# Kernel tuning notes

Measured on AMD Instinct MI355X. Metric: run time of the kernel, lower is better.

## Reference

```python
import jax, jax.numpy as jnp
import numpy as np

U1 = 512
U2 = 512
BATCH = 8192
INPUT_DIM = (U1 + U2) * 3  # 3072
UNITS = U2 * 3             # 1536


def _build_mask():
    """Replicates the block-structured random 0/1 unit_diags construction.

    Unit blocks (rows): [0,U2), [U2,2U2), [2U2,3U2).
    Input blocks (cols): ds1,ds2,ds3 of width U1 each, then stn1,stn2,stn3 of width U2.
    Each (unit-block, input-block) pair has a fixed Bernoulli keep-probability
    derived from the original randint(2)/randint(4) logic.
    """
    rng = np.random.default_rng(0)
    col_edges = [0, U1, 2 * U1, 3 * U1, 3 * U1 + U2, 3 * U1 + 2 * U2, 3 * U1 + 3 * U2]
    # keep-probabilities per unit-block (rows) x input-block (cols)
    probs = [
        [1.0, 0.5, 0.0, 1.0, 0.5, 0.0],   # units [0, U2)
        [0.5, 0.75, 0.5, 0.5, 0.75, 0.5], # units [U2, 2U2): randint(4)>0 -> p=0.75
        [0.0, 0.5, 1.0, 0.0, 0.5, 1.0],   # units [2U2, 3U2)
    ]
    p = np.zeros((UNITS, INPUT_DIM), dtype=np.float32)
    for ub in range(3):
        for j in range(6):
            p[ub * U2:(ub + 1) * U2, col_edges[j]:col_edges[j + 1]] = probs[ub][j]
    mask = (rng.random((UNITS, INPUT_DIM)) < p).astype(np.float32)
    return mask


def setup_inputs() -> dict:
    key = jax.random.key(0)
    k1, k2 = jax.random.split(key)
    x = jax.random.normal(k1, (BATCH, INPUT_DIM), dtype=jnp.float32)
    # w_init = uniform(0, 0.01), non-negative constrained
    w = jax.random.uniform(k2, (INPUT_DIM, UNITS), dtype=jnp.float32, minval=0.0, maxval=0.01)
    # gpi_bias = [0, 0] -> bias initialized to zeros
    b = jnp.zeros((UNITS,), dtype=jnp.float32)
    mask = jnp.asarray(_build_mask())  # (UNITS, INPUT_DIM), fixed 0/1 constants
    return {"x": x, "w": w, "b": b, "mask": mask}


def reference(x, w, b, mask):
    # Original: p[b,u,:] = mask[u,:] * x[b,:] ;  f = diag_part(p @ w) + b
    # => f[b,u] = sum_i mask[u,i] * x[b,i] * w[i,u] + b[u]
    # Collapses to a masked linear: x @ (mask.T * w) + b
    return x @ (mask.T * w) + b
```

## Files before the change

kernel.cpp:

```cpp
#include <hip/hip_runtime.h>
#include <stdint.h>

#define MDIM 8192
#define NDIM 1536
#define KDIM 3072

#define BM 128
#define BN 128
#define BK 64

#define NMB ((KDIM / 64) * (NDIM / 64))
#define NCVT ((MDIM * KDIM / 4) / 256)

typedef unsigned short u16;
typedef float  f32x4  __attribute__((ext_vector_type(4)));
typedef __bf16 bf16x8 __attribute__((ext_vector_type(8)));

__device__ __forceinline__ u16 f2bf(float f) {
    union { float f; unsigned int u; } v; v.f = f;
    unsigned int u = v.u;
    return (u16)((u + 0x7fffu + ((u >> 16) & 1u)) >> 16);
}

__global__ void prep_kernel(const float* __restrict__ w, const float* __restrict__ mask,
                            u16* __restrict__ Bt,
                            const float4* __restrict__ x, ushort4* __restrict__ xb) {
    const int t = threadIdx.x;
    if (blockIdx.x < NMB) {
        __shared__ float sw[64][65];
        const int kb = blockIdx.x % (KDIM / 64);
        const int nb = blockIdx.x / (KDIM / 64);
        const int k0 = kb * 64, n0 = nb * 64;
        {
            const int c4 = t & 15;
            const int r  = t >> 4;
#pragma unroll
            for (int rr = 0; rr < 4; ++rr) {
                int row = rr * 16 + r;
                float4 v = *(const float4*)&w[(size_t)(k0 + row) * NDIM + n0 + c4 * 4];
                sw[row][c4 * 4 + 0] = v.x;
                sw[row][c4 * 4 + 1] = v.y;
                sw[row][c4 * 4 + 2] = v.z;
                sw[row][c4 * 4 + 3] = v.w;
            }
        }
        __syncthreads();
        {
            const int n  = t >> 2;
            const int ks = (t & 3) * 16;
#pragma unroll
            for (int j = 0; j < 4; ++j) {
                int k = ks + j * 4;
                float4 mv = *(const float4*)&mask[(size_t)(n0 + n) * KDIM + k0 + k];
                ushort4 o;
                o.x = f2bf(mv.x * sw[k + 0][n]);
                o.y = f2bf(mv.y * sw[k + 1][n]);
                o.z = f2bf(mv.z * sw[k + 2][n]);
                o.w = f2bf(mv.w * sw[k + 3][n]);
                *(ushort4*)&Bt[(size_t)(n0 + n) * KDIM + k0 + k] = o;
            }
        }
    } else {
        int i = (blockIdx.x - NMB) * 256 + t;
        float4 v = x[i];
        ushort4 o;
        o.x = f2bf(v.x); o.y = f2bf(v.y); o.z = f2bf(v.z); o.w = f2bf(v.w);
        xb[i] = o;
    }
}

__device__ __forceinline__ void gload_lds16(const void* g, void* l) {
    __builtin_amdgcn_global_load_lds(
        (const __attribute__((address_space(1))) unsigned int*)g,
        (__attribute__((address_space(3))) unsigned int*)l, 16, 0, 0);
}

#define PLANE (128 * 32)

__global__ void gemm_kernel(const u16* __restrict__ A,
                            const u16* __restrict__ B,
                            const float* __restrict__ bias,
                            float* __restrict__ C) {
    __shared__ u16 sA[2 * PLANE];
    __shared__ u16 sB[2 * PLANE];

    const int tid  = threadIdx.x;
    const int wave = tid >> 6;
    const int lane = tid & 63;

    const int bx = blockIdx.x % (NDIM / BN);
    const int by = blockIdx.x / (NDIM / BN);
    const int m0 = by * BM, n0 = bx * BN;

    const int srow = lane >> 2;
    const int scol = ((lane & 3) ^ ((lane >> 3) & 3)) * 8;

    const int wm = (wave >> 1) * 64;
    const int wn = (wave & 1) * 64;
    const int fr = lane & 15;
    const int fq = lane >> 4;
    const int fsw = (fq ^ ((fr >> 1) & 3)) * 8;

    f32x4 acc[4][4] = {};

    const u16* gA0 = A + (size_t)(m0 + wave * 16 + srow) * KDIM + scol;
    const u16* gB0 = B + (size_t)(n0 + wave * 16 + srow) * KDIM + scol;
    u16* lA00 = &sA[0 * PLANE + (wave * 16) * 32];
    u16* lA01 = &sA[0 * PLANE + (wave * 16 + 64) * 32];
    u16* lA10 = &sA[1 * PLANE + (wave * 16) * 32];
    u16* lA11 = &sA[1 * PLANE + (wave * 16 + 64) * 32];
    u16* lB00 = &sB[0 * PLANE + (wave * 16) * 32];
    u16* lB01 = &sB[0 * PLANE + (wave * 16 + 64) * 32];
    u16* lB10 = &sB[1 * PLANE + (wave * 16) * 32];
    u16* lB11 = &sB[1 * PLANE + (wave * 16 + 64) * 32];

    for (int k0 = 0; k0 < KDIM; k0 += BK) {
        __syncthreads();
        gload_lds16(gA0 + k0,                           lA00);
        gload_lds16(gA0 + k0 + (size_t)64 * KDIM,       lA01);
        gload_lds16(gA0 + k0 + 32,                      lA10);
        gload_lds16(gA0 + k0 + 32 + (size_t)64 * KDIM,  lA11);
        gload_lds16(gB0 + k0,                           lB00);
        gload_lds16(gB0 + k0 + (size_t)64 * KDIM,       lB01);
        gload_lds16(gB0 + k0 + 32,                      lB10);
        gload_lds16(gB0 + k0 + 32 + (size_t)64 * KDIM,  lB11);
        __syncthreads();

#pragma unroll
        for (int h = 0; h < 2; ++h) {
            const u16* pA = &sA[h * PLANE];
            const u16* pB = &sB[h * PLANE];
            bf16x8 af[4], bfv[4];
#pragma unroll
            for (int mt = 0; mt < 4; ++mt)
                af[mt] = *(const bf16x8*)&pA[(wm + mt * 16 + fr) * 32 + fsw];
#pragma unroll
            for (int nt = 0; nt < 4; ++nt)
                bfv[nt] = *(const bf16x8*)&pB[(wn + nt * 16 + fr) * 32 + fsw];
#pragma unroll
            for (int mt = 0; mt < 4; ++mt)
#pragma unroll
                for (int nt = 0; nt < 4; ++nt)
                    acc[mt][nt] = __builtin_amdgcn_mfma_f32_16x16x32_bf16(
                        af[mt], bfv[nt], acc[mt][nt], 0, 0, 0);
        }
    }

#pragma unroll
    for (int nt = 0; nt < 4; ++nt) {
        int n = n0 + wn + nt * 16 + fr;
        float bv = bias[n];
#pragma unroll
        for (int mt = 0; mt < 4; ++mt) {
            int m = m0 + wm + mt * 16 + fq * 4;
#pragma unroll
            for (int r = 0; r < 4; ++r)
                C[(size_t)(m + r) * NDIM + n] = acc[mt][nt][r] + bv;
        }
    }
}

extern "C" void kernel_launch(void* const* d_in, const int* in_sizes, int n_in,
                              void* d_out, int out_size, void* d_ws, size_t ws_size,
                              hipStream_t stream) {
    const float* x    = (const float*)d_in[0];
    const float* w    = (const float*)d_in[1];
    const float* bias = (const float*)d_in[2];
    const float* mask = (const float*)d_in[3];
    float* out = (float*)d_out;

    u16* xb = (u16*)d_ws;
    u16* Bt = (u16*)((char*)d_ws + (size_t)50331648);

    prep_kernel<<<NMB + NCVT, 256, 0, stream>>>(w, mask, Bt, (const float4*)x, (ushort4*)xb);
    gemm_kernel<<<(MDIM / BM) * (NDIM / BN), 256, 0, stream>>>(xb, Bt, bias, out);
}
```

Before: 283.9 us.

## Fuse x fp32-to-bf16 conversion into GEMM A-tile loading with register prefetch

Stops pre-converting x to a bf16 workspace copy in the prep kernel. The GEMM now reads fp32 x directly into registers one tile ahead, converts to bf16 and writes into swizzled LDS, while B still streams through global_load_lds. This removes the separate write and re-read of a 48MB bf16 copy of x. In exchange x is read as fp32 once per N-tile (12 times), the A path costs extra registers and VALU work, and launch bounds are set to 3 blocks per CU.

```diff
diff --git a/kernel.cpp b/kernel.cpp
--- a/kernel.cpp
+++ b/kernel.cpp
@@ -9,11 +9,9 @@
 #define BN 128
 #define BK 64
 
-#define NMB ((KDIM / 64) * (NDIM / 64))
-#define NCVT ((MDIM * KDIM / 4) / 256)
-
 typedef unsigned short u16;
 typedef float  f32x4  __attribute__((ext_vector_type(4)));
+typedef __bf16 bf16x4 __attribute__((ext_vector_type(4)));
 typedef __bf16 bf16x8 __attribute__((ext_vector_type(8)));
 
 __device__ __forceinline__ u16 f2bf(float f) {
@@ -22,50 +20,41 @@
     return (u16)((u + 0x7fffu + ((u >> 16) & 1u)) >> 16);
 }
 
-__global__ void prep_kernel(const float* __restrict__ w, const float* __restrict__ mask,
-                            u16* __restrict__ Bt,
-                            const float4* __restrict__ x, ushort4* __restrict__ xb) {
-    const int t = threadIdx.x;
-    if (blockIdx.x < NMB) {
-        __shared__ float sw[64][65];
-        const int kb = blockIdx.x % (KDIM / 64);
-        const int nb = blockIdx.x / (KDIM / 64);
-        const int k0 = kb * 64, n0 = nb * 64;
-        {
-            const int c4 = t & 15;
-            const int r  = t >> 4;
+__global__ void make_b_kernel(const float* __restrict__ w, const float* __restrict__ mask,
+                              u16* __restrict__ Bt) {
+    __shared__ float sw[64][65];
+    const int t  = threadIdx.x;
+    const int kb = blockIdx.x % (KDIM / 64);
+    const int nb = blockIdx.x / (KDIM / 64);
+    const int k0 = kb * 64, n0 = nb * 64;
+    {
+        const int c4 = t & 15;
+        const int r  = t >> 4;
 #pragma unroll
-            for (int rr = 0; rr < 4; ++rr) {
-                int row = rr * 16 + r;
-                float4 v = *(const float4*)&w[(size_t)(k0 + row) * NDIM + n0 + c4 * 4];
-                sw[row][c4 * 4 + 0] = v.x;
-                sw[row][c4 * 4 + 1] = v.y;
-                sw[row][c4 * 4 + 2] = v.z;
-                sw[row][c4 * 4 + 3] = v.w;
-            }
+        for (int rr = 0; rr < 4; ++rr) {
+            int row = rr * 16 + r;
+            float4 v = *(const float4*)&w[(size_t)(k0 + row) * NDIM + n0 + c4 * 4];
+            sw[row][c4 * 4 + 0] = v.x;
+            sw[row][c4 * 4 + 1] = v.y;
+            sw[row][c4 * 4 + 2] = v.z;
+            sw[row][c4 * 4 + 3] = v.w;
         }
-        __syncthreads();
-        {
-            const int n  = t >> 2;
-            const int ks = (t & 3) * 16;
+    }
+    __syncthreads();
+    {
+        const int n  = t >> 2;
+        const int ks = (t & 3) * 16;
 #pragma unroll
-            for (int j = 0; j < 4; ++j) {
-                int k = ks + j * 4;
-                float4 mv = *(const float4*)&mask[(size_t)(n0 + n) * KDIM + k0 + k];
-                ushort4 o;
-                o.x = f2bf(mv.x * sw[k + 0][n]);
-                o.y = f2bf(mv.y * sw[k + 1][n]);
-                o.z = f2bf(mv.z * sw[k + 2][n]);
-                o.w = f2bf(mv.w * sw[k + 3][n]);
-                *(ushort4*)&Bt[(size_t)(n0 + n) * KDIM + k0 + k] = o;
-            }
+        for (int j = 0; j < 4; ++j) {
+            int k = ks + j * 4;
+            float4 mv = *(const float4*)&mask[(size_t)(n0 + n) * KDIM + k0 + k];
+            ushort4 o;
+            o.x = f2bf(mv.x * sw[k + 0][n]);
+            o.y = f2bf(mv.y * sw[k + 1][n]);
+            o.z = f2bf(mv.z * sw[k + 2][n]);
+            o.w = f2bf(mv.w * sw[k + 3][n]);
+            *(ushort4*)&Bt[(size_t)(n0 + n) * KDIM + k0 + k] = o;
         }
-    } else {
-        int i = (blockIdx.x - NMB) * 256 + t;
-        float4 v = x[i];
-        ushort4 o;
-        o.x = f2bf(v.x); o.y = f2bf(v.y); o.z = f2bf(v.z); o.w = f2bf(v.w);
-        xb[i] = o;
     }
 }
 
@@ -75,12 +64,13 @@
         (__attribute__((address_space(3))) unsigned int*)l, 16, 0, 0);
 }
 
-#define PLANE (128 * 32)
+#define PLANE 4096
 
-__global__ void gemm_kernel(const u16* __restrict__ A,
-                            const u16* __restrict__ B,
-                            const float* __restrict__ bias,
-                            float* __restrict__ C) {
+__global__ void __launch_bounds__(256, 3)
+gemm_kernel(const float* __restrict__ X,
+            const u16* __restrict__ B,
+            const float* __restrict__ bias,
+            float* __restrict__ C) {
     __shared__ u16 sA[2 * PLANE];
     __shared__ u16 sB[2 * PLANE];
 
@@ -92,8 +82,12 @@
     const int by = blockIdx.x / (NDIM / BN);
     const int m0 = by * BM, n0 = bx * BN;
 
-    const int srow = lane >> 2;
-    const int scol = ((lane & 3) ^ ((lane >> 3) & 3)) * 8;
+    const int aq   = lane >> 3;
+    const int ac   = lane & 7;
+    const int lds_a = (wave * 32 + aq) * 32 + (((ac >> 1) ^ (lane >> 4)) * 8) + (ac & 1) * 4;
+
+    const int bsrow = lane >> 2;
+    const int bscol = ((lane & 3) ^ ((lane >> 3) & 3)) * 8;
 
     const int wm = (wave >> 1) * 64;
     const int wn = (wave & 1) * 64;
@@ -103,27 +97,44 @@
 
     f32x4 acc[4][4] = {};
 
-    const u16* gA0 = A + (size_t)(m0 + wave * 16 + srow) * KDIM + scol;
-    const u16* gB0 = B + (size_t)(n0 + wave * 16 + srow) * KDIM + scol;
-    u16* lA00 = &sA[0 * PLANE + (wave * 16) * 32];
-    u16* lA01 = &sA[0 * PLANE + (wave * 16 + 64) * 32];
-    u16* lA10 = &sA[1 * PLANE + (wave * 16) * 32];
-    u16* lA11 = &sA[1 * PLANE + (wave * 16 + 64) * 32];
+    const float* gA = X + (size_t)(m0 + wave * 32 + aq) * KDIM + ac * 4;
+    const u16*   gB0 = B + (size_t)(n0 + wave * 16 + bsrow) * KDIM + bscol;
     u16* lB00 = &sB[0 * PLANE + (wave * 16) * 32];
     u16* lB01 = &sB[0 * PLANE + (wave * 16 + 64) * 32];
     u16* lB10 = &sB[1 * PLANE + (wave * 16) * 32];
     u16* lB11 = &sB[1 * PLANE + (wave * 16 + 64) * 32];
 
+    f32x4 ar[8];
+#pragma unroll
+    for (int p = 0; p < 2; ++p)
+#pragma unroll
+        for (int j = 0; j < 4; ++j)
+            ar[p * 4 + j] = *(const f32x4*)&gA[(size_t)(j * 8) * KDIM + p * 32];
+
     for (int k0 = 0; k0 < KDIM; k0 += BK) {
         __syncthreads();
-        gload_lds16(gA0 + k0,                           lA00);
-        gload_lds16(gA0 + k0 + (size_t)64 * KDIM,       lA01);
-        gload_lds16(gA0 + k0 + 32,                      lA10);
-        gload_lds16(gA0 + k0 + 32 + (size_t)64 * KDIM,  lA11);
+#pragma unroll
+        for (int p = 0; p < 2; ++p)
+#pragma unroll
+            for (int j = 0; j < 4; ++j) {
+                f32x4 v = ar[p * 4 + j];
+                bf16x4 o;
+#pragma unroll
+                for (int e = 0; e < 4; ++e) o[e] = (__bf16)v[e];
+                *(bf16x4*)&sA[p * PLANE + j * 256 + lds_a] = o;
+            }
         gload_lds16(gB0 + k0,                           lB00);
         gload_lds16(gB0 + k0 + (size_t)64 * KDIM,       lB01);
         gload_lds16(gB0 + k0 + 32,                      lB10);
         gload_lds16(gB0 + k0 + 32 + (size_t)64 * KDIM,  lB11);
+        if (k0 + BK < KDIM) {
+            const float* gAn = gA + k0 + BK;
+#pragma unroll
+            for (int p = 0; p < 2; ++p)
+#pragma unroll
+                for (int j = 0; j < 4; ++j)
+                    ar[p * 4 + j] = *(const f32x4*)&gAn[(size_t)(j * 8) * KDIM + p * 32];
+        }
         __syncthreads();
 
 #pragma unroll
@@ -169,9 +180,8 @@
     const float* mask = (const float*)d_in[3];
     float* out = (float*)d_out;
 
-    u16* xb = (u16*)d_ws;
-    u16* Bt = (u16*)((char*)d_ws + (size_t)50331648);
+    u16* Bt = (u16*)d_ws;
 
-    prep_kernel<<<NMB + NCVT, 256, 0, stream>>>(w, mask, Bt, (const float4*)x, (ushort4*)xb);
-    gemm_kernel<<<(MDIM / BM) * (NDIM / BN), 256, 0, stream>>>(xb, Bt, bias, out);
+    make_b_kernel<<<(KDIM / 64) * (NDIM / 64), 256, 0, stream>>>(w, mask, Bt);
+    gemm_kernel<<<(MDIM / BM) * (NDIM / BN), 256, 0, stream>>>(x, Bt, bias, out);
 }
```

Measured after the change: 294.8 us. 1.04x slower.

## Widen GEMM K-tile to 96, add launch bounds and grouped block swizzle

Applied to the files above, without the earlier changes.

The K tile grows from 64 to 96 (three 32-wide LDS planes), so the loop needs fewer synchronization round-trips per K. The block index mapping is changed so that consecutive blocks walk along M for a fixed N column in groups, which is meant to improve L2 reuse of B. Launch bounds request three blocks per CU. The risks are more LDS per block (48KB) and possible register pressure under the occupancy hint.

```diff
diff --git a/kernel.cpp b/kernel.cpp
--- a/kernel.cpp
+++ b/kernel.cpp
@@ -7,7 +7,7 @@
 
 #define BM 128
 #define BN 128
-#define BK 64
+#define BK 96
 
 #define NMB ((KDIM / 64) * (NDIM / 64))
 #define NCVT ((MDIM * KDIM / 4) / 256)
@@ -75,21 +75,23 @@
         (__attribute__((address_space(3))) unsigned int*)l, 16, 0, 0);
 }
 
-#define PLANE (128 * 32)
+#define PLANE 4096
 
-__global__ void gemm_kernel(const u16* __restrict__ A,
-                            const u16* __restrict__ B,
-                            const float* __restrict__ bias,
-                            float* __restrict__ C) {
-    __shared__ u16 sA[2 * PLANE];
-    __shared__ u16 sB[2 * PLANE];
+__global__ void __launch_bounds__(256, 3)
+gemm_kernel(const u16* __restrict__ A,
+            const u16* __restrict__ B,
+            const float* __restrict__ bias,
+            float* __restrict__ C) {
+    __shared__ u16 sA[3 * PLANE];
+    __shared__ u16 sB[3 * PLANE];
 
     const int tid  = threadIdx.x;
     const int wave = tid >> 6;
     const int lane = tid & 63;
 
-    const int bx = blockIdx.x % (NDIM / BN);
-    const int by = blockIdx.x / (NDIM / BN);
+    const int bik = blockIdx.x;
+    const int by  = (bik & 7) * 8 + ((bik >> 3) & 7);
+    const int bx  = bik >> 6;
     const int m0 = by * BM, n0 = bx * BN;
 
     const int srow = lane >> 2;
@@ -105,29 +107,24 @@
 
     const u16* gA0 = A + (size_t)(m0 + wave * 16 + srow) * KDIM + scol;
     const u16* gB0 = B + (size_t)(n0 + wave * 16 + srow) * KDIM + scol;
-    u16* lA00 = &sA[0 * PLANE + (wave * 16) * 32];
-    u16* lA01 = &sA[0 * PLANE + (wave * 16 + 64) * 32];
-    u16* lA10 = &sA[1 * PLANE + (wave * 16) * 32];
-    u16* lA11 = &sA[1 * PLANE + (wave * 16 + 64) * 32];
-    u16* lB00 = &sB[0 * PLANE + (wave * 16) * 32];
-    u16* lB01 = &sB[0 * PLANE + (wave * 16 + 64) * 32];
-    u16* lB10 = &sB[1 * PLANE + (wave * 16) * 32];
-    u16* lB11 = &sB[1 * PLANE + (wave * 16 + 64) * 32];
+    u16* lA0 = &sA[(wave * 16) * 32];
+    u16* lA1 = &sA[(wave * 16 + 64) * 32];
+    u16* lB0 = &sB[(wave * 16) * 32];
+    u16* lB1 = &sB[(wave * 16 + 64) * 32];
 
     for (int k0 = 0; k0 < KDIM; k0 += BK) {
         __syncthreads();
-        gload_lds16(gA0 + k0,                           lA00);
-        gload_lds16(gA0 + k0 + (size_t)64 * KDIM,       lA01);
-        gload_lds16(gA0 + k0 + 32,                      lA10);
-        gload_lds16(gA0 + k0 + 32 + (size_t)64 * KDIM,  lA11);
-        gload_lds16(gB0 + k0,                           lB00);
-        gload_lds16(gB0 + k0 + (size_t)64 * KDIM,       lB01);
-        gload_lds16(gB0 + k0 + 32,                      lB10);
-        gload_lds16(gB0 + k0 + 32 + (size_t)64 * KDIM,  lB11);
+#pragma unroll
+        for (int p = 0; p < 3; ++p) {
+            gload_lds16(gA0 + k0 + p * 32,                      lA0 + p * PLANE);
+            gload_lds16(gA0 + k0 + p * 32 + (size_t)64 * KDIM,  lA1 + p * PLANE);
+            gload_lds16(gB0 + k0 + p * 32,                      lB0 + p * PLANE);
+            gload_lds16(gB0 + k0 + p * 32 + (size_t)64 * KDIM,  lB1 + p * PLANE);
+        }
         __syncthreads();
 
 #pragma unroll
-        for (int h = 0; h < 2; ++h) {
+        for (int h = 0; h < 3; ++h) {
             const u16* pA = &sA[h * PLANE];
             const u16* pB = &sB[h * PLANE];
             bf16x8 af[4], bfv[4];
```

After: 281.5 us. About the same (-0.8%).
